# Kernel tuning notes

Hardware: AMD Instinct MI355X
Metric: run time of the kernel (lower is better)

The kernel has to match this reference:

```python
import jax, jax.numpy as jnp
import numpy as np

B = 8192
ITEM_NUM = 10000


def setup_inputs() -> dict:
    key = jax.random.key(0)
    k1, k2, k3, k4, k5, k6 = jax.random.split(key, 6)
    hidden_states = jax.random.normal(k1, (B, ITEM_NUM), dtype=jnp.float32)
    targetQs_s = jax.random.normal(k2, (B, ITEM_NUM), dtype=jnp.float32)
    rewards = jax.random.uniform(k3, (B,), dtype=jnp.float32)
    actions = jax.random.randint(k4, (B,), 0, ITEM_NUM)
    is_done = jnp.zeros((B,), dtype=bool)
    discount = jnp.ones((), dtype=jnp.float32) * 0.99
    # fc = nn.Linear(item_num, 1): weight [1, item_num], bias [1]
    bound = 1.0 / np.sqrt(ITEM_NUM)
    W = jax.random.uniform(k5, (1, ITEM_NUM), minval=-bound, maxval=bound, dtype=jnp.float32)
    b = jax.random.uniform(k6, (1,), minval=-bound, maxval=bound, dtype=jnp.float32)
    return {
        "hidden_states": hidden_states,
        "actions": actions,
        "rewards": rewards,
        "discount": discount,
        "targetQs_s": targetQs_s,
        "is_done": is_done,
        "W": W,
        "b": b,
    }


def reference(hidden_states, actions, rewards, discount, targetQs_s, is_done, W, b):
    # Batched equivalent of the per-sample loop:
    # q_i = relu(fc(state_i)); nq_i = relu(fc(next_state_i))
    # loss_i = |reward_i + discount * nq_i - q_i| for non-done samples
    q = jax.nn.relu(jnp.einsum('bi,oi->bo', hidden_states, W) + b)[:, 0]   # [B]
    nq = jax.nn.relu(jnp.einsum('bi,oi->bo', targetQs_s, W) + b)[:, 0]     # [B]
    per_sample = jnp.abs(rewards + discount * nq - q)                      # [B]
    total = jnp.sum(jnp.where(is_done, jnp.float32(0.0), per_sample))
    return total / hidden_states.shape[0]
```

## Files before the change

kernel.cpp:

```cpp
#include <hip/hip_runtime.h>

#define ROWS 8192
#define COLS 10000
#define COLS4 (COLS / 4)
#define BLK 256

typedef float vf4 __attribute__((ext_vector_type(4)));

__device__ __forceinline__ float dot4(vf4 a, vf4 b) {
    return a.x * b.x + a.y * b.y + a.z * b.z + a.w * b.w;
}

__global__ __launch_bounds__(BLK) void qloss_rows_kernel(
    const float* __restrict__ hidden,
    const float* __restrict__ target,
    const float* __restrict__ rewards,
    const float* __restrict__ discount,
    const unsigned char* __restrict__ is_done,
    const float* __restrict__ W,
    const float* __restrict__ bias,
    float* __restrict__ partial)
{
    const int tid  = threadIdx.x;
    const int lane = tid & 63;
    const int wid  = tid >> 6;
    const int row  = blockIdx.x;

    const vf4* __restrict__ h4 = (const vf4*)(hidden + (size_t)row * COLS);
    const vf4* __restrict__ t4 = (const vf4*)(target + (size_t)row * COLS);
    const vf4* __restrict__ w4 = (const vf4*)W;

    float ah0 = 0.f, ah1 = 0.f, at0 = 0.f, at1 = 0.f;
    int j = tid;
    for (int k = 0; k < 4; ++k, j += 512) {
        vf4 w0 = w4[j];
        vf4 w1 = w4[j + 256];
        vf4 h0 = __builtin_nontemporal_load(&h4[j]);
        vf4 h1 = __builtin_nontemporal_load(&h4[j + 256]);
        vf4 t0 = __builtin_nontemporal_load(&t4[j]);
        vf4 t1 = __builtin_nontemporal_load(&t4[j + 256]);
        ah0 += dot4(h0, w0);
        ah1 += dot4(h1, w1);
        at0 += dot4(t0, w0);
        at1 += dot4(t1, w1);
    }
    {
        vf4 w0 = w4[j];
        vf4 h0 = __builtin_nontemporal_load(&h4[j]);
        vf4 t0 = __builtin_nontemporal_load(&t4[j]);
        ah0 += dot4(h0, w0);
        at0 += dot4(t0, w0);
    }
    if (tid < COLS4 - 2304) {
        int j2 = 2304 + tid;
        vf4 w1 = w4[j2];
        vf4 h1 = __builtin_nontemporal_load(&h4[j2]);
        vf4 t1 = __builtin_nontemporal_load(&t4[j2]);
        ah1 += dot4(h1, w1);
        at1 += dot4(t1, w1);
    }

    float ah = ah0 + ah1;
    float at = at0 + at1;

    #pragma unroll
    for (int off = 32; off > 0; off >>= 1) {
        ah += __shfl_down(ah, off, 64);
        at += __shfl_down(at, off, 64);
    }

    __shared__ float smh[BLK / 64];
    __shared__ float smt[BLK / 64];
    if (lane == 0) { smh[wid] = ah; smt[wid] = at; }
    __syncthreads();

    if (tid == 0) {
        float AH = smh[0] + smh[1] + smh[2] + smh[3];
        float AT = smt[0] + smt[1] + smt[2] + smt[3];
        float b  = bias[0];
        float q  = fmaxf(AH + b, 0.f);
        float nq = fmaxf(AT + b, 0.f);
        float loss = fabsf(rewards[row] + discount[0] * nq - q);
        partial[row] = is_done[row] ? 0.f : loss;
    }
}

__global__ __launch_bounds__(BLK) void qloss_reduce_kernel(
    const float* __restrict__ partial,
    float* __restrict__ out)
{
    float s = 0.f;
    for (int i = threadIdx.x; i < ROWS; i += BLK) s += partial[i];

    #pragma unroll
    for (int off = 32; off > 0; off >>= 1) s += __shfl_down(s, off, 64);

    __shared__ float sm[BLK / 64];
    const int lane = threadIdx.x & 63;
    const int wid  = threadIdx.x >> 6;
    if (lane == 0) sm[wid] = s;
    __syncthreads();

    if (threadIdx.x == 0) {
        float total = sm[0] + sm[1] + sm[2] + sm[3];
        out[0] = total / (float)ROWS;
    }
}

extern "C" void kernel_launch(void* const* d_in, const int* in_sizes, int n_in,
                              void* d_out, int out_size, void* d_ws, size_t ws_size,
                              hipStream_t stream) {
    const float*         hidden   = (const float*)d_in[0];
    const float*         rewards  = (const float*)d_in[2];
    const float*         discount = (const float*)d_in[3];
    const float*         target   = (const float*)d_in[4];
    const unsigned char* is_done  = (const unsigned char*)d_in[5];
    const float*         W        = (const float*)d_in[6];
    const float*         b        = (const float*)d_in[7];
    float*               out      = (float*)d_out;
    float*               partial  = (float*)d_ws;

    qloss_rows_kernel<<<ROWS, BLK, 0, stream>>>(
        hidden, target, rewards, discount, is_done, W, b, partial);
    qloss_reduce_kernel<<<1, BLK, 0, stream>>>(partial, out);
}
```

Baseline: 588.0 us.

## Process eight rows per block with W held in registers

Each block now handles eight rows instead of one. The weight vector slice is loaded once into registers and reused for every row, and the per-row wave reductions are deferred into shared memory before a single sync. This cuts redundant W loads and per-block launch and sync overhead, at the cost of higher register use and fewer blocks (1024), which may reduce memory-level parallelism on a bandwidth-bound kernel.

```diff
diff --git a/kernel.cpp b/kernel.cpp
--- a/kernel.cpp
+++ b/kernel.cpp
@@ -4,6 +4,9 @@
 #define COLS 10000
 #define COLS4 (COLS / 4)
 #define BLK 256
+#define ROWS_PER_BLK 8
+#define NBLOCKS (ROWS / ROWS_PER_BLK)
+#define TAIL (COLS4 - 2304)
 
 typedef float vf4 __attribute__((ext_vector_type(4)));
 
@@ -11,7 +14,7 @@
     return a.x * b.x + a.y * b.y + a.z * b.z + a.w * b.w;
 }
 
-__global__ __launch_bounds__(BLK) void qloss_rows_kernel(
+__global__ __launch_bounds__(BLK, 4) void qloss_rows_kernel(
     const float* __restrict__ hidden,
     const float* __restrict__ target,
     const float* __restrict__ rewards,
@@ -24,59 +27,92 @@
     const int tid  = threadIdx.x;
     const int lane = tid & 63;
     const int wid  = tid >> 6;
-    const int row  = blockIdx.x;
 
-    const vf4* __restrict__ h4 = (const vf4*)(hidden + (size_t)row * COLS);
-    const vf4* __restrict__ t4 = (const vf4*)(target + (size_t)row * COLS);
     const vf4* __restrict__ w4 = (const vf4*)W;
+    vf4 wr0 = w4[tid];
+    vf4 wr1 = w4[tid + 256];
+    vf4 wr2 = w4[tid + 512];
+    vf4 wr3 = w4[tid + 768];
+    vf4 wr4 = w4[tid + 1024];
+    vf4 wr5 = w4[tid + 1280];
+    vf4 wr6 = w4[tid + 1536];
+    vf4 wr7 = w4[tid + 1792];
+    vf4 wr8 = w4[tid + 2048];
+    vf4 wr9 = {0.f, 0.f, 0.f, 0.f};
+    if (tid < TAIL) wr9 = w4[tid + 2304];
 
-    float ah0 = 0.f, ah1 = 0.f, at0 = 0.f, at1 = 0.f;
-    int j = tid;
-    for (int k = 0; k < 4; ++k, j += 512) {
-        vf4 w0 = w4[j];
-        vf4 w1 = w4[j + 256];
-        vf4 h0 = __builtin_nontemporal_load(&h4[j]);
-        vf4 h1 = __builtin_nontemporal_load(&h4[j + 256]);
-        vf4 t0 = __builtin_nontemporal_load(&t4[j]);
-        vf4 t1 = __builtin_nontemporal_load(&t4[j + 256]);
-        ah0 += dot4(h0, w0);
-        ah1 += dot4(h1, w1);
-        at0 += dot4(t0, w0);
-        at1 += dot4(t1, w1);
-    }
-    {
-        vf4 w0 = w4[j];
-        vf4 h0 = __builtin_nontemporal_load(&h4[j]);
-        vf4 t0 = __builtin_nontemporal_load(&t4[j]);
-        ah0 += dot4(h0, w0);
-        at0 += dot4(t0, w0);
-    }
-    if (tid < COLS4 - 2304) {
-        int j2 = 2304 + tid;
-        vf4 w1 = w4[j2];
-        vf4 h1 = __builtin_nontemporal_load(&h4[j2]);
-        vf4 t1 = __builtin_nontemporal_load(&t4[j2]);
-        ah1 += dot4(h1, w1);
-        at1 += dot4(t1, w1);
+    __shared__ float smh[4][ROWS_PER_BLK];
+    __shared__ float smt[4][ROWS_PER_BLK];
+
+    const int row0 = blockIdx.x * ROWS_PER_BLK;
+
+    for (int r = 0; r < ROWS_PER_BLK; ++r) {
+        const int row = row0 + r;
+        const vf4* __restrict__ h4 = (const vf4*)(hidden + (size_t)row * COLS);
+        const vf4* __restrict__ t4 = (const vf4*)(target + (size_t)row * COLS);
+
+        float ah0 = 0.f, ah1 = 0.f, at0 = 0.f, at1 = 0.f;
+        {
+            vf4 h0 = __builtin_nontemporal_load(&h4[tid]);
+            vf4 h1 = __builtin_nontemporal_load(&h4[tid + 256]);
+            vf4 t0 = __builtin_nontemporal_load(&t4[tid]);
+            vf4 t1 = __builtin_nontemporal_load(&t4[tid + 256]);
+            ah0 += dot4(h0, wr0); ah1 += dot4(h1, wr1);
+            at0 += dot4(t0, wr0); at1 += dot4(t1, wr1);
+        }
+        {
+            vf4 h0 = __builtin_nontemporal_load(&h4[tid + 512]);
+            vf4 h1 = __builtin_nontemporal_load(&h4[tid + 768]);
+            vf4 t0 = __builtin_nontemporal_load(&t4[tid + 512]);
+            vf4 t1 = __builtin_nontemporal_load(&t4[tid + 768]);
+            ah0 += dot4(h0, wr2); ah1 += dot4(h1, wr3);
+            at0 += dot4(t0, wr2); at1 += dot4(t1, wr3);
+        }
+        {
+            vf4 h0 = __builtin_nontemporal_load(&h4[tid + 1024]);
+            vf4 h1 = __builtin_nontemporal_load(&h4[tid + 1280]);
+            vf4 t0 = __builtin_nontemporal_load(&t4[tid + 1024]);
+            vf4 t1 = __builtin_nontemporal_load(&t4[tid + 1280]);
+            ah0 += dot4(h0, wr4); ah1 += dot4(h1, wr5);
+            at0 += dot4(t0, wr4); at1 += dot4(t1, wr5);
+        }
+        {
+            vf4 h0 = __builtin_nontemporal_load(&h4[tid + 1536]);
+            vf4 h1 = __builtin_nontemporal_load(&h4[tid + 1792]);
+            vf4 t0 = __builtin_nontemporal_load(&t4[tid + 1536]);
+            vf4 t1 = __builtin_nontemporal_load(&t4[tid + 1792]);
+            ah0 += dot4(h0, wr6); ah1 += dot4(h1, wr7);
+            at0 += dot4(t0, wr6); at1 += dot4(t1, wr7);
+        }
+        {
+            vf4 h0 = __builtin_nontemporal_load(&h4[tid + 2048]);
+            vf4 t0 = __builtin_nontemporal_load(&t4[tid + 2048]);
+            ah0 += dot4(h0, wr8);
+            at0 += dot4(t0, wr8);
+        }
+        if (tid < TAIL) {
+            vf4 h1 = __builtin_nontemporal_load(&h4[tid + 2304]);
+            vf4 t1 = __builtin_nontemporal_load(&t4[tid + 2304]);
+            ah1 += dot4(h1, wr9);
+            at1 += dot4(t1, wr9);
+        }
+
+        float ah = ah0 + ah1;
+        float at = at0 + at1;
+        #pragma unroll
+        for (int off = 32; off > 0; off >>= 1) {
+            ah += __shfl_down(ah, off, 64);
+            at += __shfl_down(at, off, 64);
+        }
+        if (lane == 0) { smh[wid][r] = ah; smt[wid][r] = at; }
     }
 
-    float ah = ah0 + ah1;
-    float at = at0 + at1;
-
-    #pragma unroll
-    for (int off = 32; off > 0; off >>= 1) {
-        ah += __shfl_down(ah, off, 64);
-        at += __shfl_down(at, off, 64);
-    }
-
-    __shared__ float smh[BLK / 64];
-    __shared__ float smt[BLK / 64];
-    if (lane == 0) { smh[wid] = ah; smt[wid] = at; }
     __syncthreads();
 
-    if (tid == 0) {
-        float AH = smh[0] + smh[1] + smh[2] + smh[3];
-        float AT = smt[0] + smt[1] + smt[2] + smt[3];
+    if (tid < ROWS_PER_BLK) {
+        const int row = row0 + tid;
+        float AH = smh[0][tid] + smh[1][tid] + smh[2][tid] + smh[3][tid];
+        float AT = smt[0][tid] + smt[1][tid] + smt[2][tid] + smt[3][tid];
         float b  = bias[0];
         float q  = fmaxf(AH + b, 0.f);
         float nq = fmaxf(AT + b, 0.f);
@@ -120,7 +156,7 @@
     float*               out      = (float*)d_out;
     float*               partial  = (float*)d_ws;
 
-    qloss_rows_kernel<<<ROWS, BLK, 0, stream>>>(
+    qloss_rows_kernel<<<NBLOCKS, BLK, 0, stream>>>(
         hidden, target, rewards, discount, is_done, W, b, partial);
     qloss_reduce_kernel<<<1, BLK, 0, stream>>>(partial, out);
 }
```

Result: no change. 590.7 us (+0.5%).
